# Optimization experiments

Measured on AMD Instinct MI355X. Metric: run time of the kernel, lower is better.

## Reference

```python
import jax, jax.numpy as jnp
import numpy as np

TWO_PI = 2.0 * np.pi
DT = 0.01            # self.dt buffer
COE_D, COE_M = 2, 8  # interp_degree, interp_mesh_size (per dim) for coe fitters
NL_D, NL_M = 4, 40   # nonlinear fitter degree / mesh_size
NL_A, NL_B = -15.0, 15.0  # nonlinear_interp_mesh_bound


def lagrange_basis(t, d):
    """Degree-d Lagrange basis at local coord t in [0,1]; returns [..., d+1]."""
    nodes = jnp.arange(d + 1, dtype=t.dtype) / d
    basis = []
    for j in range(d + 1):
        L = jnp.ones_like(t)
        for k in range(d + 1):
            if k != j:
                L = L * (t - nodes[k]) / (nodes[j] - nodes[k])
        basis.append(L)
    return jnp.stack(basis, axis=-1)


def interp_cells(x, a, b, m, d):
    """Map x to (cell index [..,], basis values [.., d+1]) on an m-cell mesh over [a,b]."""
    s = (x - a) / (b - a) * m
    cell = jnp.clip(jnp.floor(s), 0, m - 1)
    t = s - cell  # allows extrapolation outside [a,b] via edge cells
    return cell.astype(jnp.int32), lagrange_basis(t, d)


def nonlinear_interp(w, x):
    """1D piecewise-Lagrange fitter applied elementwise (nonlinearfitter)."""
    cell, L = interp_cells(x, NL_A, NL_B, NL_M, NL_D)
    idx = cell[..., None] * NL_D + jnp.arange(NL_D + 1)
    return jnp.sum(w[idx] * L, axis=-1)


def coe_fields(ws, xy):
    """2D tensor-product Lagrange interp on fixed inputs xy -> [C,H,W] coef fields."""
    c0, L0 = interp_cells(xy[..., 0], 0.0, TWO_PI, COE_M, COE_D)
    c1, L1 = interp_cells(xy[..., 1], 0.0, TWO_PI, COE_M, COE_D)
    i0 = c0[..., None] * COE_D + jnp.arange(COE_D + 1)   # [H,W,d+1]
    i1 = c1[..., None] * COE_D + jnp.arange(COE_D + 1)
    wloc = ws[:, i0[..., :, None], i1[..., None, :]]     # [C,H,W,d+1,d+1]
    return jnp.einsum('chwij,hwi,hwj->chw', wloc, L0, L1)


def conv_same(u, k):
    """u: [B,H,W], k: [N,1,kh,kw] -> [B,N,H,W] with zero (Dirichlet) padding."""
    return jax.lax.conv_general_dilated(u[:, None], k, (1, 1), 'SAME',
                                        dimension_numbers=('NCHW', 'OIHW', 'NCHW'))


def setup_inputs() -> dict:
    key = jax.random.key(0)
    ks = jax.random.split(key, 5)
    B, H, W, K, N = 16, 512, 512, 5, 6
    init = jax.random.normal(ks[0], (B, H, W), jnp.float32)
    delta = jnp.zeros((1, 1, K, K), jnp.float32).at[0, 0, K // 2, K // 2].set(1.0)
    idkernel = delta + 0.01 * jax.random.normal(ks[1], (1, 1, K, K), jnp.float32)
    fdkernel = 0.1 * jax.random.normal(ks[2], (N, 1, K, K), jnp.float32)
    M = COE_M * COE_D + 1
    coe_w = 0.1 * jax.random.normal(ks[3], (N - 1, M, M), jnp.float32)
    nl_w = 0.1 * jax.random.normal(ks[4], (NL_M * NL_D + 1,), jnp.float32)
    gx = jnp.linspace(0.0, TWO_PI, H, endpoint=False).astype(jnp.float32)
    xy = jnp.stack(jnp.meshgrid(gx, gx, indexing='ij'), axis=-1)  # [H,W,2]
    return {"init": init, "idkernel": idkernel, "fdkernel": fdkernel,
            "coe_w": coe_w, "nl_w": nl_w, "xy": xy, "stepnum": 8}


def reference(init, idkernel, fdkernel, coe_w, nl_w, xy, stepnum):
    # coefficient fields are evaluated once (fixed xy), as in the torch forward
    coe = coe_fields(coe_w, xy)[None]  # [1, N-1, H, W], broadcasts over batch

    def step(u, _):
        uid = conv_same(u, idkernel)[:, 0]           # [B,H,W]
        ufd = conv_same(u, fdkernel)                 # [B,N,H,W]
        un = uid + DT * ((coe * ufd[:, 1:]).sum(axis=1)
                         + nonlinear_interp(nl_w, ufd[:, 0]))
        return un, None

    u, _ = jax.lax.scan(step, init, None, length=stepnum)
    return u
```

## Files before the change

kernel.cpp:

```cpp
#include <hip/hip_runtime.h>

typedef float f2 __attribute__((ext_vector_type(2)));

static constexpr int HH = 512;
static constexpr int WW = 512;
static constexpr int HW = HH * WW;
static constexpr int NB = 16;
static constexpr float DT_F = 0.01f;
static constexpr float TWO_PI_F = 6.283185307179586f;
static constexpr int STEPS = 8;

static constexpr int TW = 64;
static constexpr int TH = 16;
static constexpr int LW = 72;
static constexpr int LH = TH + 4;

__device__ const float NLM[5][5] = {
    {1.0f,      -25.0f/3.0f,   70.0f/3.0f,  -80.0f/3.0f,   32.0f/3.0f},
    {0.0f,       16.0f,      -208.0f/3.0f,   96.0f,      -128.0f/3.0f},
    {0.0f,      -12.0f,        76.0f,      -128.0f,        64.0f},
    {0.0f,   16.0f/3.0f,    -112.0f/3.0f,  224.0f/3.0f, -128.0f/3.0f},
    {0.0f,      -1.0f,       22.0f/3.0f,   -16.0f,        32.0f/3.0f},
};

__device__ __forceinline__ void pkfma_s(f2& acc, f2 w, f2 u) {
    asm("v_pk_fma_f32 %0, %1, %2, %0" : "+v"(acc) : "s"(w), "v"(u));
}
__device__ __forceinline__ void pkfma_v(f2& acc, f2 a, f2 b) {
    asm("v_pk_fma_f32 %0, %1, %2, %0" : "+v"(acc) : "v"(a), "v"(b));
}

__global__ __launch_bounds__(256) void coe_kernel(const float* __restrict__ coe_w,
                                                  const float* __restrict__ xy,
                                                  float* __restrict__ coe)
{
    __shared__ float sw[5 * 17 * 17];
    for (int i = threadIdx.x; i < 5 * 17 * 17; i += 256) sw[i] = coe_w[i];
    __syncthreads();

    int p = blockIdx.x * 256 + threadIdx.x;
    if (p >= HW) return;

    float x0 = xy[2 * p + 0];
    float x1 = xy[2 * p + 1];

    float s0 = x0 / TWO_PI_F * 8.0f;
    float c0f = fminf(fmaxf(floorf(s0), 0.0f), 7.0f);
    float t0 = s0 - c0f;
    int i0 = 2 * (int)c0f;

    float s1 = x1 / TWO_PI_F * 8.0f;
    float c1f = fminf(fmaxf(floorf(s1), 0.0f), 7.0f);
    float t1 = s1 - c1f;
    int i1 = 2 * (int)c1f;

    float L0[3], L1[3];
    L0[0] = (t0 - 0.5f) * (t0 - 1.0f) * 2.0f;
    L0[1] = t0 * (t0 - 1.0f) * -4.0f;
    L0[2] = t0 * (t0 - 0.5f) * 2.0f;
    L1[0] = (t1 - 0.5f) * (t1 - 1.0f) * 2.0f;
    L1[1] = t1 * (t1 - 1.0f) * -4.0f;
    L1[2] = t1 * (t1 - 0.5f) * 2.0f;

    #pragma unroll
    for (int c = 0; c < 5; ++c) {
        float acc = 0.0f;
        #pragma unroll
        for (int i = 0; i < 3; ++i) {
            #pragma unroll
            for (int j = 0; j < 3; ++j) {
                acc = fmaf(sw[c * 289 + (i0 + i) * 17 + (i1 + j)], L0[i] * L1[j], acc);
            }
        }
        coe[c * HW + p] = acc;
    }
}

__global__ __launch_bounds__(256) void step_kernel(
    const float* __restrict__ uin,
    float* __restrict__ uout,
    const float* __restrict__ kid,
    const float* __restrict__ kfd,
    const float* __restrict__ nlw,
    const float* __restrict__ coe)
{
    __shared__ float su[LH][LW];
    __shared__ float snlp[40 * 8];

    const int tid = threadIdx.x;
    const int bx = blockIdx.x & 7;
    const int by = (blockIdx.x >> 3) & 31;
    const int b  = blockIdx.x >> 8;
    const int col0 = bx * TW;
    const int row0 = by * TH;
    const float* ub = uin + b * HW;

    if (tid < 200) {
        const int c = tid / 5;
        const int m = tid - 5 * c;
        float a = nlw[4 * c + 0] * NLM[0][m];
        a = fmaf(nlw[4 * c + 1], NLM[1][m], a);
        a = fmaf(nlw[4 * c + 2], NLM[2][m], a);
        a = fmaf(nlw[4 * c + 3], NLM[3][m], a);
        a = fmaf(nlw[4 * c + 4], NLM[4][m], a);
        snlp[c * 8 + m] = a;
    }

    for (int it = tid; it < LH * 18; it += 256) {
        const int lr = it / 18;
        const int j  = it - lr * 18;
        const int gr = row0 - 2 + lr;
        const int gc = col0 - 4 + 4 * j;
        float4 v = make_float4(0.f, 0.f, 0.f, 0.f);
        if (gr >= 0 && gr < HH && gc >= 0 && gc + 3 < WW)
            v = *reinterpret_cast<const float4*>(ub + gr * WW + gc);
        if (j == 0) {
            *reinterpret_cast<float2*>(&su[lr][0]) = make_float2(v.z, v.w);
        } else if (j == 17) {
            *reinterpret_cast<float2*>(&su[lr][66]) = make_float2(v.x, v.y);
        } else {
            const int lc = 4 * j - 2;
            *reinterpret_cast<float2*>(&su[lr][lc])     = make_float2(v.x, v.y);
            *reinterpret_cast<float2*>(&su[lr][lc + 2]) = make_float2(v.z, v.w);
        }
    }
    __syncthreads();

    const int t16 = tid & 15;
    const int tyr = tid >> 4;
    const int c4  = t16 * 4;
    const int p   = (row0 + tyr) * WW + col0 + c4;

    float4 coev[5];
    #pragma unroll
    for (int n = 0; n < 5; ++n)
        coev[n] = *reinterpret_cast<const float4*>(&coe[n * HW + p]);

    f2 accid2[2];
    f2 accf2[6][2];
    accid2[0] = (f2){0.f, 0.f}; accid2[1] = (f2){0.f, 0.f};
    #pragma unroll
    for (int n = 0; n < 6; ++n) {
        accf2[n][0] = (f2){0.f, 0.f};
        accf2[n][1] = (f2){0.f, 0.f};
    }

    #pragma unroll
    for (int dy = 0; dy < 5; ++dy) {
        const float4 w0 = *reinterpret_cast<const float4*>(&su[tyr + dy][c4]);
        const float4 w1 = *reinterpret_cast<const float4*>(&su[tyr + dy][c4 + 4]);
        const f2 r01 = (f2){w0.x, w0.y};
        const f2 r23 = (f2){w0.z, w0.w};
        const f2 r45 = (f2){w1.x, w1.y};
        const f2 r67 = (f2){w1.z, w1.w};
        const f2 r12 = (f2){w0.y, w0.z};
        const f2 r34 = (f2){w0.w, w1.x};
        const f2 r56 = (f2){w1.y, w1.z};

        #define CONV_DX(DX, PL, PH)                                          \
        {                                                                     \
            const int o = dy * 5 + (DX);                                      \
            f2 wv;                                                            \
            wv.x = kid[o];       wv.y = wv.x;                                 \
            pkfma_s(accid2[0],   wv, PL); pkfma_s(accid2[1],   wv, PH);       \
            wv.x = kfd[o];       wv.y = wv.x;                                 \
            pkfma_s(accf2[0][0], wv, PL); pkfma_s(accf2[0][1], wv, PH);       \
            wv.x = kfd[25 + o];  wv.y = wv.x;                                 \
            pkfma_s(accf2[1][0], wv, PL); pkfma_s(accf2[1][1], wv, PH);       \
            wv.x = kfd[50 + o];  wv.y = wv.x;                                 \
            pkfma_s(accf2[2][0], wv, PL); pkfma_s(accf2[2][1], wv, PH);       \
            wv.x = kfd[75 + o];  wv.y = wv.x;                                 \
            pkfma_s(accf2[3][0], wv, PL); pkfma_s(accf2[3][1], wv, PH);       \
            wv.x = kfd[100 + o]; wv.y = wv.x;                                 \
            pkfma_s(accf2[4][0], wv, PL); pkfma_s(accf2[4][1], wv, PH);       \
            wv.x = kfd[125 + o]; wv.y = wv.x;                                 \
            pkfma_s(accf2[5][0], wv, PL); pkfma_s(accf2[5][1], wv, PH);       \
        }
        CONV_DX(0, r01, r23)
        CONV_DX(1, r12, r34)
        CONV_DX(2, r23, r45)
        CONV_DX(3, r34, r56)
        CONV_DX(4, r45, r67)
        #undef CONV_DX
    }

    f2 cs2[2];
    cs2[0] = (f2){0.f, 0.f}; cs2[1] = (f2){0.f, 0.f};
    #pragma unroll
    for (int n = 0; n < 5; ++n) {
        const f2 c01 = (f2){coev[n].x, coev[n].y};
        const f2 c23 = (f2){coev[n].z, coev[n].w};
        pkfma_v(cs2[0], c01, accf2[n + 1][0]);
        pkfma_v(cs2[1], c23, accf2[n + 1][1]);
    }

    const float xs[4]  = {accf2[0][0].x, accf2[0][0].y, accf2[0][1].x, accf2[0][1].y};
    const float csv[4] = {cs2[0].x, cs2[0].y, cs2[1].x, cs2[1].y};
    const float idv[4] = {accid2[0].x, accid2[0].y, accid2[1].x, accid2[1].y};

    float outv[4];
    #pragma unroll
    for (int k = 0; k < 4; ++k) {
        const float x = xs[k];
        const float sc = fmaf(x, 4.0f / 3.0f, 20.0f);
        const float cf = fminf(fmaxf(floorf(sc), 0.0f), 39.0f);
        const float t = sc - cf;
        const int base = (int)cf * 8;
        const float4 cm = *reinterpret_cast<const float4*>(&snlp[base]);
        const float cm4 = snlp[base + 4];
        float r = fmaf(cm4, t, cm.w);
        r = fmaf(r, t, cm.z);
        r = fmaf(r, t, cm.y);
        r = fmaf(r, t, cm.x);
        outv[k] = fmaf(DT_F, csv[k] + r, idv[k]);
    }

    *reinterpret_cast<float4*>(&uout[b * HW + p]) =
        make_float4(outv[0], outv[1], outv[2], outv[3]);
}

extern "C" void kernel_launch(void* const* d_in, const int* in_sizes, int n_in,
                              void* d_out, int out_size, void* d_ws, size_t ws_size,
                              hipStream_t stream)
{
    const float* init = (const float*)d_in[0];
    const float* idk  = (const float*)d_in[1];
    const float* fdk  = (const float*)d_in[2];
    const float* coew = (const float*)d_in[3];
    const float* nlw  = (const float*)d_in[4];
    const float* xy   = (const float*)d_in[5];

    float* ws  = (float*)d_ws;
    float* coe = ws;
    float* uA  = coe + 5 * HW;
    float* uB  = uA + NB * HW;

    coe_kernel<<<(HW + 255) / 256, 256, 0, stream>>>(coew, xy, coe);

    const int nblk = NB * (HH / TH) * (WW / TW);
    const float* src = init;
    for (int s = 0; s < STEPS; ++s) {
        float* dst = (s == STEPS - 1) ? (float*)d_out : ((s & 1) ? uB : uA);
        step_kernel<<<nblk, 256, 0, stream>>>(src, dst, idk, fdk, nlw, coe);
        src = dst;
    }
}
```

Before: 188.5 us.

## Load stencil window directly into registers instead of staging through LDS

Removes the shared-memory tile for u and has each thread load its own 5x12 halo window straight from global memory into registers, with a fast interior path and a bounds-checked edge path. It also replaces the packed v_pk_fma inline assembly with plain scalar fmaf loops that the compiler schedules itself. The aim is to drop the LDS store/load traffic and its bank pressure. The cost is redundant global and L2 reads of the overlapping halo rows (about 3.75x), more registers per thread, and losing the packed FMA throughput.

```diff
diff --git a/kernel.cpp b/kernel.cpp
--- a/kernel.cpp
+++ b/kernel.cpp
@@ -1,6 +1,4 @@
 #include <hip/hip_runtime.h>
-
-typedef float f2 __attribute__((ext_vector_type(2)));
 
 static constexpr int HH = 512;
 static constexpr int WW = 512;
@@ -12,8 +10,6 @@
 
 static constexpr int TW = 64;
 static constexpr int TH = 16;
-static constexpr int LW = 72;
-static constexpr int LH = TH + 4;
 
 __device__ const float NLM[5][5] = {
     {1.0f,      -25.0f/3.0f,   70.0f/3.0f,  -80.0f/3.0f,   32.0f/3.0f},
@@ -22,13 +18,6 @@
     {0.0f,   16.0f/3.0f,    -112.0f/3.0f,  224.0f/3.0f, -128.0f/3.0f},
     {0.0f,      -1.0f,       22.0f/3.0f,   -16.0f,        32.0f/3.0f},
 };
-
-__device__ __forceinline__ void pkfma_s(f2& acc, f2 w, f2 u) {
-    asm("v_pk_fma_f32 %0, %1, %2, %0" : "+v"(acc) : "s"(w), "v"(u));
-}
-__device__ __forceinline__ void pkfma_v(f2& acc, f2 a, f2 b) {
-    asm("v_pk_fma_f32 %0, %1, %2, %0" : "+v"(acc) : "v"(a), "v"(b));
-}
 
 __global__ __launch_bounds__(256) void coe_kernel(const float* __restrict__ coe_w,
                                                   const float* __restrict__ xy,
@@ -84,7 +73,6 @@
     const float* __restrict__ nlw,
     const float* __restrict__ coe)
 {
-    __shared__ float su[LH][LW];
     __shared__ float snlp[40 * 8];
 
     const int tid = threadIdx.x;
@@ -94,6 +82,39 @@
     const int col0 = bx * TW;
     const int row0 = by * TH;
     const float* ub = uin + b * HW;
+
+    const int t16 = tid & 15;
+    const int tyr = tid >> 4;
+    const int c4  = t16 * 4;
+    const int grow = row0 + tyr;
+    const int gcol = col0 + c4;
+
+    float4 win4[5][3];
+    const bool interior = (row0 >= 2) & (row0 + TH + 2 <= HH) & (bx > 0) & (bx < 7);
+    if (interior) {
+        const float* wp = ub + (grow - 2) * WW + gcol - 4;
+        #pragma unroll
+        for (int dy = 0; dy < 5; ++dy) {
+            win4[dy][0] = *reinterpret_cast<const float4*>(wp);
+            win4[dy][1] = *reinterpret_cast<const float4*>(wp + 4);
+            win4[dy][2] = *reinterpret_cast<const float4*>(wp + 8);
+            wp += WW;
+        }
+    } else {
+        #pragma unroll
+        for (int dy = 0; dy < 5; ++dy) {
+            const int gr = grow - 2 + dy;
+            const bool rowok = (gr >= 0) & (gr < HH);
+            #pragma unroll
+            for (int j = 0; j < 3; ++j) {
+                const int gc = gcol - 4 + 4 * j;
+                float4 v = make_float4(0.f, 0.f, 0.f, 0.f);
+                if (rowok & (gc >= 0) & (gc + 3 < WW))
+                    v = *reinterpret_cast<const float4*>(ub + gr * WW + gc);
+                win4[dy][j] = v;
+            }
+        }
+    }
 
     if (tid < 200) {
         const int c = tid / 5;
@@ -105,103 +126,69 @@
         a = fmaf(nlw[4 * c + 4], NLM[4][m], a);
         snlp[c * 8 + m] = a;
     }
-
-    for (int it = tid; it < LH * 18; it += 256) {
-        const int lr = it / 18;
-        const int j  = it - lr * 18;
-        const int gr = row0 - 2 + lr;
-        const int gc = col0 - 4 + 4 * j;
-        float4 v = make_float4(0.f, 0.f, 0.f, 0.f);
-        if (gr >= 0 && gr < HH && gc >= 0 && gc + 3 < WW)
-            v = *reinterpret_cast<const float4*>(ub + gr * WW + gc);
-        if (j == 0) {
-            *reinterpret_cast<float2*>(&su[lr][0]) = make_float2(v.z, v.w);
-        } else if (j == 17) {
-            *reinterpret_cast<float2*>(&su[lr][66]) = make_float2(v.x, v.y);
-        } else {
-            const int lc = 4 * j - 2;
-            *reinterpret_cast<float2*>(&su[lr][lc])     = make_float2(v.x, v.y);
-            *reinterpret_cast<float2*>(&su[lr][lc + 2]) = make_float2(v.z, v.w);
-        }
-    }
     __syncthreads();
 
-    const int t16 = tid & 15;
-    const int tyr = tid >> 4;
-    const int c4  = t16 * 4;
-    const int p   = (row0 + tyr) * WW + col0 + c4;
-
+    const int p = grow * WW + gcol;
     float4 coev[5];
     #pragma unroll
     for (int n = 0; n < 5; ++n)
         coev[n] = *reinterpret_cast<const float4*>(&coe[n * HW + p]);
 
-    f2 accid2[2];
-    f2 accf2[6][2];
-    accid2[0] = (f2){0.f, 0.f}; accid2[1] = (f2){0.f, 0.f};
-    #pragma unroll
-    for (int n = 0; n < 6; ++n) {
-        accf2[n][0] = (f2){0.f, 0.f};
-        accf2[n][1] = (f2){0.f, 0.f};
-    }
-
+    float accid[4] = {0.f, 0.f, 0.f, 0.f};
+    float accf[6][4];
+    #pragma unroll
+    for (int n = 0; n < 6; ++n)
+        #pragma unroll
+        for (int k = 0; k < 4; ++k) accf[n][k] = 0.f;
+
+    const float* win = reinterpret_cast<const float*>(win4);
     #pragma unroll
     for (int dy = 0; dy < 5; ++dy) {
-        const float4 w0 = *reinterpret_cast<const float4*>(&su[tyr + dy][c4]);
-        const float4 w1 = *reinterpret_cast<const float4*>(&su[tyr + dy][c4 + 4]);
-        const f2 r01 = (f2){w0.x, w0.y};
-        const f2 r23 = (f2){w0.z, w0.w};
-        const f2 r45 = (f2){w1.x, w1.y};
-        const f2 r67 = (f2){w1.z, w1.w};
-        const f2 r12 = (f2){w0.y, w0.z};
-        const f2 r34 = (f2){w0.w, w1.x};
-        const f2 r56 = (f2){w1.y, w1.z};
-
-        #define CONV_DX(DX, PL, PH)                                          \
-        {                                                                     \
-            const int o = dy * 5 + (DX);                                      \
-            f2 wv;                                                            \
-            wv.x = kid[o];       wv.y = wv.x;                                 \
-            pkfma_s(accid2[0],   wv, PL); pkfma_s(accid2[1],   wv, PH);       \
-            wv.x = kfd[o];       wv.y = wv.x;                                 \
-            pkfma_s(accf2[0][0], wv, PL); pkfma_s(accf2[0][1], wv, PH);       \
-            wv.x = kfd[25 + o];  wv.y = wv.x;                                 \
-            pkfma_s(accf2[1][0], wv, PL); pkfma_s(accf2[1][1], wv, PH);       \
-            wv.x = kfd[50 + o];  wv.y = wv.x;                                 \
-            pkfma_s(accf2[2][0], wv, PL); pkfma_s(accf2[2][1], wv, PH);       \
-            wv.x = kfd[75 + o];  wv.y = wv.x;                                 \
-            pkfma_s(accf2[3][0], wv, PL); pkfma_s(accf2[3][1], wv, PH);       \
-            wv.x = kfd[100 + o]; wv.y = wv.x;                                 \
-            pkfma_s(accf2[4][0], wv, PL); pkfma_s(accf2[4][1], wv, PH);       \
-            wv.x = kfd[125 + o]; wv.y = wv.x;                                 \
-            pkfma_s(accf2[5][0], wv, PL); pkfma_s(accf2[5][1], wv, PH);       \
-        }
-        CONV_DX(0, r01, r23)
-        CONV_DX(1, r12, r34)
-        CONV_DX(2, r23, r45)
-        CONV_DX(3, r34, r56)
-        CONV_DX(4, r45, r67)
-        #undef CONV_DX
-    }
-
-    f2 cs2[2];
-    cs2[0] = (f2){0.f, 0.f}; cs2[1] = (f2){0.f, 0.f};
-    #pragma unroll
-    for (int n = 0; n < 5; ++n) {
-        const f2 c01 = (f2){coev[n].x, coev[n].y};
-        const f2 c23 = (f2){coev[n].z, coev[n].w};
-        pkfma_v(cs2[0], c01, accf2[n + 1][0]);
-        pkfma_v(cs2[1], c23, accf2[n + 1][1]);
-    }
-
-    const float xs[4]  = {accf2[0][0].x, accf2[0][0].y, accf2[0][1].x, accf2[0][1].y};
-    const float csv[4] = {cs2[0].x, cs2[0].y, cs2[1].x, cs2[1].y};
-    const float idv[4] = {accid2[0].x, accid2[0].y, accid2[1].x, accid2[1].y};
+        #pragma unroll
+        for (int dx = 0; dx < 5; ++dx) {
+            const int o = dy * 5 + dx;
+            const float w0k = kid[o];
+            const float f0 = kfd[o];
+            const float f1 = kfd[25 + o];
+            const float f2 = kfd[50 + o];
+            const float f3 = kfd[75 + o];
+            const float f4 = kfd[100 + o];
+            const float f5 = kfd[125 + o];
+            #pragma unroll
+            for (int k = 0; k < 4; ++k) {
+                const float uv = win[dy * 12 + 2 + dx + k];
+                accid[k]   = fmaf(w0k, uv, accid[k]);
+                accf[0][k] = fmaf(f0, uv, accf[0][k]);
+                accf[1][k] = fmaf(f1, uv, accf[1][k]);
+                accf[2][k] = fmaf(f2, uv, accf[2][k]);
+                accf[3][k] = fmaf(f3, uv, accf[3][k]);
+                accf[4][k] = fmaf(f4, uv, accf[4][k]);
+                accf[5][k] = fmaf(f5, uv, accf[5][k]);
+            }
+        }
+    }
+
+    float cs[4];
+    {
+        const float* cv = reinterpret_cast<const float*>(&coev[0]);
+        cs[0] = cv[0] * accf[1][0];
+        cs[1] = cv[1] * accf[1][1];
+        cs[2] = cv[2] * accf[1][2];
+        cs[3] = cv[3] * accf[1][3];
+    }
+    #pragma unroll
+    for (int n = 1; n < 5; ++n) {
+        const float* cv = reinterpret_cast<const float*>(&coev[n]);
+        cs[0] = fmaf(cv[0], accf[n + 1][0], cs[0]);
+        cs[1] = fmaf(cv[1], accf[n + 1][1], cs[1]);
+        cs[2] = fmaf(cv[2], accf[n + 1][2], cs[2]);
+        cs[3] = fmaf(cv[3], accf[n + 1][3], cs[3]);
+    }
 
     float outv[4];
     #pragma unroll
     for (int k = 0; k < 4; ++k) {
-        const float x = xs[k];
+        const float x = accf[0][k];
         const float sc = fmaf(x, 4.0f / 3.0f, 20.0f);
         const float cf = fminf(fmaxf(floorf(sc), 0.0f), 39.0f);
         const float t = sc - cf;
@@ -212,7 +199,7 @@
         r = fmaf(r, t, cm.z);
         r = fmaf(r, t, cm.y);
         r = fmaf(r, t, cm.x);
-        outv[k] = fmaf(DT_F, csv[k] + r, idv[k]);
+        outv[k] = fmaf(DT_F, cs[k] + r, accid[k]);
     }
 
     *reinterpret_cast<float4*>(&uout[b * HW + p]) =
```

Measured after the change: 210.3 us. +11.6%, slower.
